# Kernel tuning notes

Measured on AMD Instinct MI355X. Metric: run time of the kernel, lower is better.

The kernel has to match this reference:

```python
import jax, jax.numpy as jnp
import numpy as np

N_NODES = 100000
N_EDGES = 3200000
IN_CH = 256
OUT_CH = 64
HEADS = 2
NEG_SLOPE = 0.2  # PyG GATConv default


def setup_inputs() -> dict:
    key = jax.random.key(0)
    k1, k2, k3, k4, k5 = jax.random.split(key, 5)
    z = jax.random.normal(k1, (N_NODES, IN_CH), dtype=jnp.float32)
    edge_index = jax.random.randint(k2, (2, N_EDGES), 0, N_NODES, dtype=jnp.int64)
    # Glorot-ish scaled params
    W = jax.random.normal(k3, (IN_CH, HEADS * OUT_CH), dtype=jnp.float32) / np.sqrt(IN_CH)
    att_src = jax.random.normal(k4, (1, HEADS, OUT_CH), dtype=jnp.float32) / np.sqrt(OUT_CH)
    att_dst = jax.random.normal(k5, (1, HEADS, OUT_CH), dtype=jnp.float32) / np.sqrt(OUT_CH)
    bias = jnp.zeros((OUT_CH,), dtype=jnp.float32)
    return {"z": z, "edge_index": edge_index, "W": W,
            "att_src": att_src, "att_dst": att_dst, "bias": bias}


def reference(z, edge_index, W, att_src, att_dst, bias):
    # PyG GATConv forward (eval mode: attention dropout is identity),
    # add_self_loops=True, concat=False (mean over heads), no activation.
    n = z.shape[0]
    loop = jnp.arange(n, dtype=edge_index.dtype)
    src = jnp.concatenate([edge_index[0], loop])  # (Etot,)
    dst = jnp.concatenate([edge_index[1], loop])

    x = (z @ W).reshape(n, HEADS, OUT_CH)  # per-head projected features (n,H,C)
    a_src = jnp.sum(x * att_src, axis=-1)  # (n,H)
    a_dst = jnp.sum(x * att_dst, axis=-1)  # (n,H)

    logits = a_src[src] + a_dst[dst]       # (Etot,H)
    logits = jax.nn.leaky_relu(logits, NEG_SLOPE)

    # segment softmax over edges grouped by destination node
    seg_max = jax.ops.segment_max(logits, dst, num_segments=n)   # (n,H)
    e = jnp.exp(logits - seg_max[dst])
    seg_sum = jax.ops.segment_sum(e, dst, num_segments=n)        # (n,H)
    alpha = e / seg_sum[dst]                                     # (Etot,H)

    msgs = x[src] * alpha[:, :, None]                            # (Etot,H,C)
    out = jax.ops.segment_sum(msgs, dst, num_segments=n)         # (n,H,C)
    out = out.mean(axis=1) + bias                                # concat=False -> mean
    return out
```

## Files before the change

### kernel.cpp

```cpp
#include <hip/hip_runtime.h>
#include <hip/hip_bf16.h>
#include <hip/hip_fp16.h>

#define IN_CH   256
#define NOUT    128
#define OUT_CH  64
#define NEG     0.2f

#define NBINS     256
#define BIN_SHIFT 9
#define NPB       512
#define CAPB      18432
#define EPT       8

typedef __attribute__((ext_vector_type(8))) short bf16x8;
typedef __attribute__((ext_vector_type(4))) float f32x4;

static __device__ __forceinline__ short f2bf(float f) {
    __hip_bfloat16 h = __float2bfloat16(f);
    return *reinterpret_cast<short*>(&h);
}

static __device__ __forceinline__ int pack_e(float l0, float l1) {
    __half2 h2;
    h2.x = __float2half(__expf(l0));
    h2.y = __float2half(__expf(l1));
    return *reinterpret_cast<int*>(&h2);
}

__global__ void k_transpose_w(const float* __restrict__ W,
                              __hip_bfloat16* __restrict__ Wt) {
    int i = blockIdx.x * blockDim.x + threadIdx.x;
    if (i < IN_CH * NOUT) {
        int n = i >> 8, k = i & 255;
        Wt[i] = __float2bfloat16(W[k * NOUT + n]);
    }
}

__global__ __launch_bounds__(256) void k_gemm_x(
        const float* __restrict__ z,
        const __hip_bfloat16* __restrict__ wt,
        const float* __restrict__ att_s,
        const float* __restrict__ att_d,
        __hip_bfloat16* __restrict__ x,
        float* __restrict__ a_src, float* __restrict__ a_dst, int nTiles) {
    int wid  = (blockIdx.x * blockDim.x + threadIdx.x) >> 6;
    if (wid >= nTiles) return;
    int lane = threadIdx.x & 63;
    int m = lane & 15, quad = lane >> 4;
    int rbase = wid * 16;
    const float* zp = z + (size_t)(rbase + m) * IN_CH + quad * 8;
    const short* wp = (const short*)wt + m * IN_CH + quad * 8;
    f32x4 acc[8] = {};
#pragma unroll
    for (int kb = 0; kb < 8; ++kb) {
        float4 f0 = *(const float4*)(zp + kb * 32);
        float4 f1 = *(const float4*)(zp + kb * 32 + 4);
        bf16x8 a;
        a[0] = f2bf(f0.x); a[1] = f2bf(f0.y); a[2] = f2bf(f0.z); a[3] = f2bf(f0.w);
        a[4] = f2bf(f1.x); a[5] = f2bf(f1.y); a[6] = f2bf(f1.z); a[7] = f2bf(f1.w);
#pragma unroll
        for (int n = 0; n < 8; ++n) {
            bf16x8 b = *(const bf16x8*)(wp + n * 16 * IN_CH + kb * 32);
            acc[n] = __builtin_amdgcn_mfma_f32_16x16x32_bf16(a, b, acc[n], 0, 0, 0);
        }
    }
#pragma unroll
    for (int n = 0; n < 8; ++n)
#pragma unroll
        for (int r = 0; r < 4; ++r) {
            int row = rbase + quad * 4 + r;
            x[(size_t)row * NOUT + n * 16 + m] = __float2bfloat16(acc[n][r]);
        }
    float asv[8], adv[8];
#pragma unroll
    for (int n = 0; n < 8; ++n) {
        asv[n] = att_s[n * 16 + m];
        adv[n] = att_d[n * 16 + m];
    }
    float ps0[4] = {}, ps1[4] = {}, pd0[4] = {}, pd1[4] = {};
#pragma unroll
    for (int r = 0; r < 4; ++r)
#pragma unroll
        for (int n = 0; n < 4; ++n) {
            ps0[r] += acc[n][r] * asv[n];
            ps1[r] += acc[n + 4][r] * asv[n + 4];
            pd0[r] += acc[n][r] * adv[n];
            pd1[r] += acc[n + 4][r] * adv[n + 4];
        }
#pragma unroll
    for (int msk = 1; msk < 16; msk <<= 1)
#pragma unroll
        for (int r = 0; r < 4; ++r) {
            ps0[r] += __shfl_xor(ps0[r], msk);
            ps1[r] += __shfl_xor(ps1[r], msk);
            pd0[r] += __shfl_xor(pd0[r], msk);
            pd1[r] += __shfl_xor(pd1[r], msk);
        }
    if (m < 4) {
        int r = m;
        int row = rbase + quad * 4 + r;
        ((float2*)a_src)[row] = make_float2(ps0[r], ps1[r]);
        ((float2*)a_dst)[row] = make_float2(pd0[r], pd1[r]);
    }
}

__global__ __launch_bounds__(256) void k_pass1(
        const int* __restrict__ ei,
        const float* __restrict__ a_src, const float* __restrict__ a_dst,
        int* __restrict__ gcnt, int2* __restrict__ binned, int E) {
    __shared__ int lcnt[NBINS];
    __shared__ int lptr[NBINS];
    int t = threadIdx.x;
    int base = blockIdx.x * (256 * EPT);
    if (t < NBINS) lcnt[t] = 0;
    __syncthreads();

    int2 pay[EPT];
    int  bn[EPT];
#pragma unroll
    for (int j = 0; j < EPT; ++j) {
        int e = base + j * 256 + t;
        bn[j] = -1;
        if (e < E) {
            int s = ei[e], d = ei[E + e];
            float2 as = ((const float2*)a_src)[s];
            float2 ad = ((const float2*)a_dst)[d];
            float l0 = as.x + ad.x; l0 = (l0 > 0.f) ? l0 : NEG * l0;
            float l1 = as.y + ad.y; l1 = (l1 > 0.f) ? l1 : NEG * l1;
            pay[j] = make_int2(pack_e(l0, l1), ((d & (NPB - 1)) << 17) | s);
            bn[j] = d >> BIN_SHIFT;
            atomicAdd(&lcnt[bn[j]], 1);
        }
    }
    __syncthreads();
    if (t < NBINS) {
        int c = lcnt[t];
        lptr[t] = (c > 0) ? atomicAdd(&gcnt[t], c) : 0;
    }
    __syncthreads();
#pragma unroll
    for (int j = 0; j < EPT; ++j) {
        if (bn[j] >= 0) {
            int pos = atomicAdd(&lptr[bn[j]], 1);
            if (pos < CAPB)
                binned[(size_t)bn[j] * CAPB + pos] = pay[j];
        }
    }
}

__global__ void k_binscan(const int* __restrict__ gcnt, int* __restrict__ binBase,
                          int* __restrict__ offs, int N) {
    __shared__ int sd[NBINS];
    int t = threadIdx.x;
    int nodes = N - t * NPB;
    nodes = (nodes < 0) ? 0 : ((nodes > NPB) ? NPB : nodes);
    int c = gcnt[t];
    if (c > CAPB) c = CAPB;
    int v = c + nodes;
    sd[t] = v;
    __syncthreads();
    for (int off = 1; off < NBINS; off <<= 1) {
        int u = (t >= off) ? sd[t - off] : 0;
        __syncthreads();
        sd[t] += u;
        __syncthreads();
    }
    binBase[t] = sd[t] - v;
    if (t == NBINS - 1) offs[N] = sd[t];
}

__global__ __launch_bounds__(1024) void k_pass2(
        const int2* __restrict__ binned, const int* __restrict__ gcnt,
        const int* __restrict__ binBase,
        const float* __restrict__ a_src, const float* __restrict__ a_dst,
        int2* __restrict__ epk, int* __restrict__ offs, int N) {
    __shared__ int lh[NPB];
    __shared__ int lx[NPB];
    int b = blockIdx.x, t = threadIdx.x;
    int nodes = N - b * NPB;
    nodes = (nodes < 0) ? 0 : ((nodes > NPB) ? NPB : nodes);
    if (nodes == 0) return;
    int cnt = gcnt[b];
    if (cnt > CAPB) cnt = CAPB;
    int base = binBase[b];
    const int2* src = binned + (size_t)b * CAPB;

    if (t < NPB) lh[t] = (t < nodes) ? 1 : 0;
    __syncthreads();
    for (int i = t; i < cnt; i += 1024)
        atomicAdd(&lh[(src[i].y >> 17) & (NPB - 1)], 1);
    __syncthreads();
    if (t < NPB) lx[t] = lh[t];
    __syncthreads();
    for (int off = 1; off < NPB; off <<= 1) {
        int u = (t < NPB && t >= off) ? lx[t - off] : 0;
        __syncthreads();
        if (t < NPB) lx[t] += u;
        __syncthreads();
    }
    int excl = 0;
    if (t < NPB) {
        excl = lx[t] - lh[t];
        lh[t] = excl + 1;
    }
    __syncthreads();
    if (t < nodes) {
        int d = b * NPB + t;
        float2 as = ((const float2*)a_src)[d];
        float2 ad = ((const float2*)a_dst)[d];
        float l0 = as.x + ad.x; l0 = (l0 > 0.f) ? l0 : NEG * l0;
        float l1 = as.y + ad.y; l1 = (l1 > 0.f) ? l1 : NEG * l1;
        epk[base + excl] = make_int2(pack_e(l0, l1), d);
        offs[d] = base + excl;
    }
    for (int i = t; i < cnt; i += 1024) {
        int2 p = src[i];
        int dLow = (p.y >> 17) & (NPB - 1);
        int pos = atomicAdd(&lh[dLow], 1);
        epk[base + pos] = make_int2(p.x, p.y & 0x1FFFF);
    }
}

__global__ __launch_bounds__(256) void k_gat_agg(
        const int2* __restrict__ epk, const int* __restrict__ offs,
        const __hip_bfloat16* __restrict__ x, const float* __restrict__ bias,
        float* __restrict__ out, int N) {
    int wid  = (blockIdx.x * blockDim.x + threadIdx.x) >> 6;
    if (wid >= N) return;
    int lane = threadIdx.x & 63;
    int beg = offs[wid], end = offs[wid + 1];
    int h = lane >> 5;
    const __hip_bfloat162* xv = (const __hip_bfloat162*)x;

    float ax[4] = {}, ay[4] = {}, dn[4] = {};
    int i = beg;
    for (; i + 3 < end; i += 4) {
#pragma unroll
        for (int u = 0; u < 4; ++u) {
            int2 p = epk[i + u];
            __half2 h2 = *reinterpret_cast<__half2*>(&p.x);
            float2 ef = __half22float2(h2);
            float e = h ? ef.y : ef.x;
            __hip_bfloat162 f = xv[(size_t)p.y * 64 + lane];
            ax[u] += e * __bfloat162float(f.x);
            ay[u] += e * __bfloat162float(f.y);
            dn[u] += e;
        }
    }
    for (; i < end; ++i) {
        int2 p = epk[i];
        __half2 h2 = *reinterpret_cast<__half2*>(&p.x);
        float2 ef = __half22float2(h2);
        float e = h ? ef.y : ef.x;
        __hip_bfloat162 f = xv[(size_t)p.y * 64 + lane];
        ax[0] += e * __bfloat162float(f.x);
        ay[0] += e * __bfloat162float(f.y);
        dn[0] += e;
    }
    float inv = 1.f / ((dn[0] + dn[1]) + (dn[2] + dn[3]));
    float accx = ((ax[0] + ax[1]) + (ax[2] + ax[3])) * inv;
    float accy = ((ay[0] + ay[1]) + (ay[2] + ay[3])) * inv;
    float o0 = accx + __shfl_xor(accx, 32);
    float o1 = accy + __shfl_xor(accy, 32);
    if (lane < 32) {
        int c = 2 * lane;
        float2 o;
        o.x = 0.5f * o0 + bias[c];
        o.y = 0.5f * o1 + bias[c + 1];
        ((float2*)out)[(size_t)wid * 32 + lane] = o;
    }
}

extern "C" void kernel_launch(void* const* d_in, const int* in_sizes, int n_in,
                              void* d_out, int out_size, void* d_ws, size_t ws_size,
                              hipStream_t stream) {
    const float* z     = (const float*)d_in[0];
    const int*   ei    = (const int*)d_in[1];
    const float* W     = (const float*)d_in[2];
    const float* att_s = (const float*)d_in[3];
    const float* att_d = (const float*)d_in[4];
    const float* bias  = (const float*)d_in[5];
    float* out = (float*)d_out;

    const int N = in_sizes[0] / IN_CH;
    const int E = in_sizes[1] / 2;
    const int Etot = E + N;

    size_t off = 0;
    auto alloc = [&](size_t bytes) {
        void* p = (char*)d_ws + off;
        off += (bytes + 255) & ~(size_t)255;
        return p;
    };
    __hip_bfloat16* x    = (__hip_bfloat16*)alloc((size_t)N * NOUT * 2);
    __hip_bfloat16* Wt   = (__hip_bfloat16*)alloc((size_t)IN_CH * NOUT * 2);
    float* a_src         = (float*)alloc((size_t)N * 2 * 4);
    float* a_dst         = (float*)alloc((size_t)N * 2 * 4);
    int*   gcnt          = (int*)alloc(NBINS * 4);
    int*   binBase       = (int*)alloc(NBINS * 4);
    int*   offs          = (int*)alloc((size_t)(N + 1) * 4);
    int2*  binned        = (int2*)alloc((size_t)NBINS * CAPB * 8);
    int2*  epk           = (int2*)alloc((size_t)Etot * 8);
    (void)ws_size;

    const int nTiles = N / 16;
    const int p1Blocks = (E + 256 * EPT - 1) / (256 * EPT);

    hipMemsetAsync(gcnt, 0, NBINS * 4, stream);
    k_transpose_w<<<(IN_CH * NOUT + 255) / 256, 256, 0, stream>>>(W, Wt);
    k_gemm_x<<<(nTiles + 3) / 4, 256, 0, stream>>>(z, Wt, att_s, att_d, x, a_src, a_dst, nTiles);
    k_pass1<<<p1Blocks, 256, 0, stream>>>(ei, a_src, a_dst, gcnt, binned, E);
    k_binscan<<<1, NBINS, 0, stream>>>(gcnt, binBase, offs, N);
    k_pass2<<<NBINS, 1024, 0, stream>>>(binned, gcnt, binBase, a_src, a_dst, epk, offs, N);
    k_gat_agg<<<(N + 3) / 4, 256, 0, stream>>>(epk, offs, x, bias, out, N);
}
```

Before: 442.7 us.

## Defer logit computation to pass2, shrink binned payload, drop binscan kernel

Pass1 now writes only a 4-byte packed (dst-low, src) entry per edge instead of an 8-byte payload with precomputed exp-logits. This halves the binned scratch traffic, and pass1 no longer does random a_src/a_dst gathers. Pass2 computes the logits itself, reading a_dst from shared memory and gathering a_src. It also claims its output range with a global atomic instead of a separate scan kernel, and writes begin and end offsets per node. EPT doubles to 16, and bin order in epk becomes nondeterministic, which is still correct because each node's begin and end are stored explicitly.

Measured after the change: 428.9 us. 3.1% less time.

```diff
diff --git a/kernel.cpp b/kernel.cpp
--- a/kernel.cpp
+++ b/kernel.cpp
@@ -11,7 +11,7 @@
 #define BIN_SHIFT 9
 #define NPB       512
 #define CAPB      18432
-#define EPT       8
+#define EPT       16
 
 typedef __attribute__((ext_vector_type(8))) short bf16x8;
 typedef __attribute__((ext_vector_type(4))) float f32x4;
@@ -107,34 +107,28 @@
 
 __global__ __launch_bounds__(256) void k_pass1(
         const int* __restrict__ ei,
-        const float* __restrict__ a_src, const float* __restrict__ a_dst,
-        int* __restrict__ gcnt, int2* __restrict__ binned, int E) {
+        int* __restrict__ gcnt, int* __restrict__ binned, int E) {
     __shared__ int lcnt[NBINS];
     __shared__ int lptr[NBINS];
     int t = threadIdx.x;
     int base = blockIdx.x * (256 * EPT);
-    if (t < NBINS) lcnt[t] = 0;
-    __syncthreads();
-
-    int2 pay[EPT];
-    int  bn[EPT];
+    lcnt[t] = 0;
+    __syncthreads();
+
+    int ent[EPT], bn[EPT];
 #pragma unroll
     for (int j = 0; j < EPT; ++j) {
         int e = base + j * 256 + t;
         bn[j] = -1;
         if (e < E) {
             int s = ei[e], d = ei[E + e];
-            float2 as = ((const float2*)a_src)[s];
-            float2 ad = ((const float2*)a_dst)[d];
-            float l0 = as.x + ad.x; l0 = (l0 > 0.f) ? l0 : NEG * l0;
-            float l1 = as.y + ad.y; l1 = (l1 > 0.f) ? l1 : NEG * l1;
-            pay[j] = make_int2(pack_e(l0, l1), ((d & (NPB - 1)) << 17) | s);
-            bn[j] = d >> BIN_SHIFT;
+            ent[j] = ((d & (NPB - 1)) << 17) | s;
+            bn[j]  = d >> BIN_SHIFT;
             atomicAdd(&lcnt[bn[j]], 1);
         }
     }
     __syncthreads();
-    if (t < NBINS) {
+    {
         int c = lcnt[t];
         lptr[t] = (c > 0) ? atomicAdd(&gcnt[t], c) : 0;
     }
@@ -144,52 +138,36 @@
         if (bn[j] >= 0) {
             int pos = atomicAdd(&lptr[bn[j]], 1);
             if (pos < CAPB)
-                binned[(size_t)bn[j] * CAPB + pos] = pay[j];
-        }
-    }
-}
-
-__global__ void k_binscan(const int* __restrict__ gcnt, int* __restrict__ binBase,
-                          int* __restrict__ offs, int N) {
-    __shared__ int sd[NBINS];
-    int t = threadIdx.x;
-    int nodes = N - t * NPB;
-    nodes = (nodes < 0) ? 0 : ((nodes > NPB) ? NPB : nodes);
-    int c = gcnt[t];
-    if (c > CAPB) c = CAPB;
-    int v = c + nodes;
-    sd[t] = v;
-    __syncthreads();
-    for (int off = 1; off < NBINS; off <<= 1) {
-        int u = (t >= off) ? sd[t - off] : 0;
-        __syncthreads();
-        sd[t] += u;
-        __syncthreads();
-    }
-    binBase[t] = sd[t] - v;
-    if (t == NBINS - 1) offs[N] = sd[t];
+                binned[(size_t)bn[j] * CAPB + pos] = ent[j];
+        }
+    }
 }
 
 __global__ __launch_bounds__(1024) void k_pass2(
-        const int2* __restrict__ binned, const int* __restrict__ gcnt,
-        const int* __restrict__ binBase,
+        const int* __restrict__ binned, const int* __restrict__ gcnt,
+        int* __restrict__ gtot,
         const float* __restrict__ a_src, const float* __restrict__ a_dst,
-        int2* __restrict__ epk, int* __restrict__ offs, int N) {
-    __shared__ int lh[NPB];
-    __shared__ int lx[NPB];
+        int2* __restrict__ epk, int* __restrict__ offsB, int* __restrict__ offsE, int N) {
+    __shared__ int    lh[NPB];
+    __shared__ int    lx[NPB];
+    __shared__ float2 sad[NPB];
+    __shared__ int    sBase;
     int b = blockIdx.x, t = threadIdx.x;
     int nodes = N - b * NPB;
     nodes = (nodes < 0) ? 0 : ((nodes > NPB) ? NPB : nodes);
     if (nodes == 0) return;
     int cnt = gcnt[b];
     if (cnt > CAPB) cnt = CAPB;
-    int base = binBase[b];
-    const int2* src = binned + (size_t)b * CAPB;
-
-    if (t < NPB) lh[t] = (t < nodes) ? 1 : 0;
+    const int* src = binned + (size_t)b * CAPB;
+
+    if (t == 0) sBase = atomicAdd(gtot, cnt + nodes);
+    if (t < NPB) {
+        lh[t] = (t < nodes) ? 1 : 0;
+        if (t < nodes) sad[t] = ((const float2*)a_dst)[b * NPB + t];
+    }
     __syncthreads();
     for (int i = t; i < cnt; i += 1024)
-        atomicAdd(&lh[(src[i].y >> 17) & (NPB - 1)], 1);
+        atomicAdd(&lh[(src[i] >> 17) & (NPB - 1)], 1);
     __syncthreads();
     if (t < NPB) lx[t] = lh[t];
     __syncthreads();
@@ -199,37 +177,44 @@
         if (t < NPB) lx[t] += u;
         __syncthreads();
     }
+    int base = sBase;
     int excl = 0;
-    if (t < NPB) {
-        excl = lx[t] - lh[t];
-        lh[t] = excl + 1;
-    }
+    if (t < NPB) excl = lx[t] - lh[t];
+    __syncthreads();
+    if (t < NPB) lh[t] = excl + 1;
     __syncthreads();
     if (t < nodes) {
         int d = b * NPB + t;
         float2 as = ((const float2*)a_src)[d];
-        float2 ad = ((const float2*)a_dst)[d];
+        float2 ad = sad[t];
         float l0 = as.x + ad.x; l0 = (l0 > 0.f) ? l0 : NEG * l0;
         float l1 = as.y + ad.y; l1 = (l1 > 0.f) ? l1 : NEG * l1;
         epk[base + excl] = make_int2(pack_e(l0, l1), d);
-        offs[d] = base + excl;
+        offsB[d] = base + excl;
+        offsE[d] = base + lx[t];
     }
     for (int i = t; i < cnt; i += 1024) {
-        int2 p = src[i];
-        int dLow = (p.y >> 17) & (NPB - 1);
+        int ent = src[i];
+        int dLow = (ent >> 17) & (NPB - 1);
+        int s = ent & 0x1FFFF;
+        float2 as = ((const float2*)a_src)[s];
+        float2 ad = sad[dLow];
+        float l0 = as.x + ad.x; l0 = (l0 > 0.f) ? l0 : NEG * l0;
+        float l1 = as.y + ad.y; l1 = (l1 > 0.f) ? l1 : NEG * l1;
         int pos = atomicAdd(&lh[dLow], 1);
-        epk[base + pos] = make_int2(p.x, p.y & 0x1FFFF);
+        epk[base + pos] = make_int2(pack_e(l0, l1), s);
     }
 }
 
 __global__ __launch_bounds__(256) void k_gat_agg(
-        const int2* __restrict__ epk, const int* __restrict__ offs,
+        const int2* __restrict__ epk,
+        const int* __restrict__ offsB, const int* __restrict__ offsE,
         const __hip_bfloat16* __restrict__ x, const float* __restrict__ bias,
         float* __restrict__ out, int N) {
     int wid  = (blockIdx.x * blockDim.x + threadIdx.x) >> 6;
     if (wid >= N) return;
     int lane = threadIdx.x & 63;
-    int beg = offs[wid], end = offs[wid + 1];
+    int beg = offsB[wid], end = offsE[wid];
     int h = lane >> 5;
     const __hip_bfloat162* xv = (const __hip_bfloat162*)x;
 
@@ -297,21 +282,21 @@
     __hip_bfloat16* Wt   = (__hip_bfloat16*)alloc((size_t)IN_CH * NOUT * 2);
     float* a_src         = (float*)alloc((size_t)N * 2 * 4);
     float* a_dst         = (float*)alloc((size_t)N * 2 * 4);
-    int*   gcnt          = (int*)alloc(NBINS * 4);
-    int*   binBase       = (int*)alloc(NBINS * 4);
-    int*   offs          = (int*)alloc((size_t)(N + 1) * 4);
-    int2*  binned        = (int2*)alloc((size_t)NBINS * CAPB * 8);
+    int*   gcnt          = (int*)alloc((NBINS + 1) * 4);
+    int*   gtot          = gcnt + NBINS;
+    int*   offsB         = (int*)alloc((size_t)N * 4);
+    int*   offsE         = (int*)alloc((size_t)N * 4);
+    int*   binned        = (int*)alloc((size_t)NBINS * CAPB * 4);
     int2*  epk           = (int2*)alloc((size_t)Etot * 8);
     (void)ws_size;
 
     const int nTiles = N / 16;
     const int p1Blocks = (E + 256 * EPT - 1) / (256 * EPT);
 
-    hipMemsetAsync(gcnt, 0, NBINS * 4, stream);
+    hipMemsetAsync(gcnt, 0, (NBINS + 1) * 4, stream);
     k_transpose_w<<<(IN_CH * NOUT + 255) / 256, 256, 0, stream>>>(W, Wt);
     k_gemm_x<<<(nTiles + 3) / 4, 256, 0, stream>>>(z, Wt, att_s, att_d, x, a_src, a_dst, nTiles);
-    k_pass1<<<p1Blocks, 256, 0, stream>>>(ei, a_src, a_dst, gcnt, binned, E);
-    k_binscan<<<1, NBINS, 0, stream>>>(gcnt, binBase, offs, N);
-    k_pass2<<<NBINS, 1024, 0, stream>>>(binned, gcnt, binBase, a_src, a_dst, epk, offs, N);
-    k_gat_agg<<<(N + 3) / 4, 256, 0, stream>>>(epk, offs, x, bias, out, N);
-}
+    k_pass1<<<p1Blocks, 256, 0, stream>>>(ei, gcnt, binned, E);
+    k_pass2<<<NBINS, 1024, 0, stream>>>(binned, gcnt, gtot, a_src, a_dst, epk, offsB, offsE, N);
+    k_gat_agg<<<(N + 3) / 4, 256, 0, stream>>>(epk, offsB, offsE, x, bias, out, N);
+}
```
